# Performance work log

Measured on AMD Instinct MI355X. Metric: run time of the kernel, lower is better.

## Reference

```python
import jax, jax.numpy as jnp
import numpy as np

N = 100000   # nodes
E = 1600000  # edges
F = 128      # input/hidden dim
C = 3        # classes
G = 64       # graphs in batch


def setup_inputs() -> dict:
    key = jax.random.key(0)
    ks = jax.random.split(key, 12)
    s = 1.0 / np.sqrt(F)
    return {
        "x": jax.random.normal(ks[0], (N, F), dtype=jnp.float32),
        "edge_index": jax.random.randint(ks[1], (2, E), 0, N, dtype=jnp.int64),
        "batch": jnp.sort(jax.random.randint(ks[2], (N,), 0, G, dtype=jnp.int64)),
        "W1": jax.random.normal(ks[3], (F, F), dtype=jnp.float32) * s,
        "b1": jnp.zeros((F,), dtype=jnp.float32),
        "W2": jax.random.normal(ks[4], (F, F), dtype=jnp.float32) * s,
        "b2": jnp.zeros((F,), dtype=jnp.float32),
        "W3": jax.random.normal(ks[5], (F, F), dtype=jnp.float32) * s,
        "b3": jnp.zeros((F,), dtype=jnp.float32),
        "Wc": jax.random.normal(ks[6], (F, C), dtype=jnp.float32) * s,
        "bc": jnp.zeros((C,), dtype=jnp.float32),
    }


def reference(x, edge_index, batch, W1, b1, W2, b2, W3, b3, Wc, bc):
    n = x.shape[0]
    src, dst = edge_index[0], edge_index[1]
    # GCN adds self-loops: A_hat = A + I
    loops = jnp.arange(n, dtype=src.dtype)
    src_a = jnp.concatenate([src, loops])
    dst_a = jnp.concatenate([dst, loops])
    # symmetric normalization D^-1/2 (A+I) D^-1/2 (in-degree incl. self-loop)
    deg = jax.ops.segment_sum(jnp.ones_like(dst_a, dtype=x.dtype), dst_a, num_segments=n)
    dis = jnp.where(deg > 0, jax.lax.rsqrt(deg), 0.0)
    norm = dis[src_a] * dis[dst_a]  # [E+N]

    def gcn_conv(h, W, b):
        h = h @ W                                    # [N, F']
        msg = h[src_a] * norm[:, None]               # gather + scale
        agg = jax.ops.segment_sum(msg, dst_a, num_segments=n)  # scatter-add
        return agg + b

    h = jax.nn.relu(gcn_conv(x, W1, b1))   # dropout = identity in eval mode
    h = jax.nn.relu(gcn_conv(h, W2, b2))
    h = jax.nn.relu(gcn_conv(h, W3, b3))

    # global_mean_pool over graph ids
    sums = jax.ops.segment_sum(h, batch, num_segments=G)
    cnt = jax.ops.segment_sum(jnp.ones((n,), dtype=h.dtype), batch, num_segments=G)
    pooled = sums / jnp.maximum(cnt, 1.0)[:, None]
    return pooled @ Wc + bc
```

## Files before the change

### kernel.cpp

```cpp
#include <hip/hip_runtime.h>
#include <cstdint>
#include <cstddef>

#define FDIM 128
#define CHUNK 4096
#define BSHIFT 8
#define BMASK 255
#define MAXB 512

typedef unsigned short ushort_t;
typedef __attribute__((ext_vector_type(8))) short short8;
typedef __attribute__((ext_vector_type(4))) float floatx4;

__device__ inline ushort_t f2bf(float f) {
  unsigned u = __float_as_uint(f);
  u += 0x7fffu + ((u >> 16) & 1u);
  return (ushort_t)(u >> 16);
}
__device__ inline float bf2f(ushort_t h) {
  return __uint_as_float((unsigned)h << 16);
}

__global__ __launch_bounds__(256) void k_front(
    const float* __restrict__ x, const float* __restrict__ W1,
    const float* __restrict__ W2, const float* __restrict__ W3,
    ushort_t* __restrict__ h0, int n, int mmb,
    const int* __restrict__ dst, int e, int nb,
    int* __restrict__ chunkHist, int nch,
    ushort_t* __restrict__ wsw, int* __restrict__ counter,
    float* __restrict__ partials_g, int g_count) {
  __shared__ ushort_t Bs[16384];
  int tid = threadIdx.x;
  int bid = blockIdx.x;
  if (bid >= mmb) {
    int r = bid - mmb;
    if (r < nch) {
      int* h = (int*)Bs;
      int base = r * CHUNK;
      int end = min(base + CHUNK, e);
      for (int i = tid; i < nb; i += 256) h[i] = 0;
      __syncthreads();
      for (int i = base + tid; i < end; i += 256)
        atomicAdd(&h[dst[i] >> BSHIFT], 1);
      __syncthreads();
      for (int b = tid; b < nb; b += 256)
        chunkHist[(size_t)r * nb + b] = h[b];
      return;
    }
    int b = r - nch;
    if (b == 2) {
      for (int i = tid; i < g_count * FDIM; i += 256) partials_g[i] = 0.f;
      return;
    }
    if (b == 0 && tid == 0) *counter = 0;
    const float* W = (b == 0) ? W2 : W3;
    ushort_t* o = wsw + (size_t)b * 16384;
    for (int idx = tid; idx < 16384; idx += 256) {
      int j = idx & 7;
      int lane = (idx >> 3) & 63;
      int ct = (idx >> 9) & 7;
      int kc = idx >> 12;
      int k = kc * 32 + (lane >> 4) * 8 + j;
      int col = (lane & 15) * 8 + ct;
      o[idx] = f2bf(W[k * FDIM + col]);
    }
    return;
  }
  for (int q = tid; q < 2048; q += 256) {
    int lane = q & 63;
    int ct = (q >> 6) & 7;
    int kc = q >> 9;
    int col = (lane & 15) * 8 + ct;
    int kb = kc * 32 + (lane >> 4) * 8;
    unsigned t0 = f2bf(W1[(kb + 0) * FDIM + col]);
    unsigned t1 = f2bf(W1[(kb + 1) * FDIM + col]);
    unsigned t2 = f2bf(W1[(kb + 2) * FDIM + col]);
    unsigned t3 = f2bf(W1[(kb + 3) * FDIM + col]);
    unsigned t4 = f2bf(W1[(kb + 4) * FDIM + col]);
    unsigned t5 = f2bf(W1[(kb + 5) * FDIM + col]);
    unsigned t6 = f2bf(W1[(kb + 6) * FDIM + col]);
    unsigned t7 = f2bf(W1[(kb + 7) * FDIM + col]);
    uint4 pk;
    pk.x = t0 | (t1 << 16);
    pk.y = t2 | (t3 << 16);
    pk.z = t4 | (t5 << 16);
    pk.w = t6 | (t7 << 16);
    ((uint4*)Bs)[q] = pk;
  }
  __syncthreads();

  int w = tid >> 6;
  int lane = tid & 63;
  int quad = lane >> 4;
  int l15 = lane & 15;
  int rb = bid * 128 + w * 32;
  int row0 = rb + l15;
  int row1 = rb + 16 + l15;
  bool v0 = row0 < n, v1 = row1 < n;

  floatx4 acc[2][8];
#pragma unroll
  for (int rt = 0; rt < 2; ++rt)
#pragma unroll
    for (int ct = 0; ct < 8; ++ct) acc[rt][ct] = floatx4{0.f, 0.f, 0.f, 0.f};

#pragma unroll
  for (int kc = 0; kc < 4; ++kc) {
    int k0 = kc * 32 + quad * 8;
    short8 a0 = short8{0, 0, 0, 0, 0, 0, 0, 0};
    short8 a1 = short8{0, 0, 0, 0, 0, 0, 0, 0};
    if (v0) {
      float4 f0 = *(const float4*)&x[(size_t)row0 * FDIM + k0];
      float4 f1 = *(const float4*)&x[(size_t)row0 * FDIM + k0 + 4];
      a0 = short8{(short)f2bf(f0.x), (short)f2bf(f0.y), (short)f2bf(f0.z),
                  (short)f2bf(f0.w), (short)f2bf(f1.x), (short)f2bf(f1.y),
                  (short)f2bf(f1.z), (short)f2bf(f1.w)};
    }
    if (v1) {
      float4 f0 = *(const float4*)&x[(size_t)row1 * FDIM + k0];
      float4 f1 = *(const float4*)&x[(size_t)row1 * FDIM + k0 + 4];
      a1 = short8{(short)f2bf(f0.x), (short)f2bf(f0.y), (short)f2bf(f0.z),
                  (short)f2bf(f0.w), (short)f2bf(f1.x), (short)f2bf(f1.y),
                  (short)f2bf(f1.z), (short)f2bf(f1.w)};
    }
#pragma unroll
    for (int ct = 0; ct < 8; ++ct) {
      short8 bf = *(const short8*)&Bs[((kc * 8 + ct) * 64 + lane) * 8];
      acc[0][ct] = __builtin_amdgcn_mfma_f32_16x16x32_bf16(a0, bf, acc[0][ct], 0, 0, 0);
      acc[1][ct] = __builtin_amdgcn_mfma_f32_16x16x32_bf16(a1, bf, acc[1][ct], 0, 0, 0);
    }
  }
#pragma unroll
  for (int rt = 0; rt < 2; ++rt) {
#pragma unroll
    for (int i = 0; i < 4; ++i) {
      int row = rb + rt * 16 + quad * 4 + i;
      if (row < n) {
        uint4 pk;
        pk.x = (unsigned)f2bf(acc[rt][0][i]) | ((unsigned)f2bf(acc[rt][1][i]) << 16);
        pk.y = (unsigned)f2bf(acc[rt][2][i]) | ((unsigned)f2bf(acc[rt][3][i]) << 16);
        pk.z = (unsigned)f2bf(acc[rt][4][i]) | ((unsigned)f2bf(acc[rt][5][i]) << 16);
        pk.w = (unsigned)f2bf(acc[rt][6][i]) | ((unsigned)f2bf(acc[rt][7][i]) << 16);
        *(uint4*)&h0[(size_t)row * FDIM + l15 * 8] = pk;
      }
    }
  }
}

__global__ __launch_bounds__(512) void k_scan1(const int* __restrict__ chunkHist,
                                               int nchunks, int nb,
                                               int* __restrict__ chunkOff,
                                               int* __restrict__ bucketTotal,
                                               int* __restrict__ bucketBase,
                                               int* __restrict__ counter) {
  __shared__ int sb[512];
  int b = blockIdx.x;
  int t = threadIdx.x;
  int base = 0;
  for (int c0 = 0; c0 < nchunks; c0 += 512) {
    int c = c0 + t;
    int v = (c < nchunks) ? chunkHist[(size_t)c * nb + b] : 0;
    int x = v;
    sb[t] = x;
    __syncthreads();
    for (int off = 1; off < 512; off <<= 1) {
      int y = (t >= off) ? sb[t - off] : 0;
      __syncthreads();
      x += y;
      sb[t] = x;
      __syncthreads();
    }
    if (c < nchunks) chunkOff[(size_t)c * nb + b] = base + x - v;
    int tileTot = sb[511];
    __syncthreads();
    base += tileTot;
  }
  if (t == 0) {
    bucketTotal[b] = base;
    bucketBase[b] = atomicAdd(counter, base);
  }
}

__global__ __launch_bounds__(256) void k_bin(const int* __restrict__ src,
                                             const int* __restrict__ dst, int e, int nb,
                                             const int* __restrict__ chunkHist,
                                             const int* __restrict__ chunkOff,
                                             const int* __restrict__ bucketBase,
                                             unsigned* __restrict__ binned) {
  __shared__ unsigned sortedL[CHUNK];
  __shared__ int gtarget[CHUNK];
  __shared__ int lbase[MAXB], lcur[MAXB], gbase[MAXB];
  __shared__ int stmp[256];
  int c = blockIdx.x;
  int base = c * CHUNK;
  int end = min(base + CHUNK, e);
  for (int i = threadIdx.x; i < nb; i += 256) {
    lbase[i] = chunkHist[(size_t)c * nb + i];
    gbase[i] = bucketBase[i] + chunkOff[(size_t)c * nb + i];
  }
  __syncthreads();
  int carry = 0;
  for (int i0 = 0; i0 < nb; i0 += 256) {
    int i = i0 + threadIdx.x;
    int v = (i < nb) ? lbase[i] : 0;
    int x = v;
    stmp[threadIdx.x] = x;
    __syncthreads();
    for (int off = 1; off < 256; off <<= 1) {
      int y = (threadIdx.x >= off) ? stmp[threadIdx.x - off] : 0;
      __syncthreads();
      x += y;
      stmp[threadIdx.x] = x;
      __syncthreads();
    }
    if (i < nb) lbase[i] = carry + x - v;
    int tileTot = stmp[255];
    __syncthreads();
    carry += tileTot;
  }
  for (int i = threadIdx.x; i < nb; i += 256) lcur[i] = lbase[i];
  __syncthreads();
  for (int i = base + threadIdx.x; i < end; i += 256) {
    int d = dst[i];
    int sv = src[i];
    int b = d >> BSHIFT;
    int slot = atomicAdd(&lcur[b], 1);
    sortedL[slot] = ((unsigned)sv << BSHIFT) | (unsigned)(d & BMASK);
    gtarget[slot] = gbase[b] + (slot - lbase[b]);
  }
  __syncthreads();
  for (int i = threadIdx.x; i < end - base; i += 256)
    binned[gtarget[i]] = sortedL[i];
}

__global__ __launch_bounds__(256) void k_fill2(const unsigned* __restrict__ binned,
                                               const int* __restrict__ bucketBase,
                                               const int* __restrict__ bucketTotal,
                                               int n,
                                               int* __restrict__ rowStart,
                                               int* __restrict__ deg,
                                               float* __restrict__ dis,
                                               unsigned* __restrict__ colPacked) {
  __shared__ int h[256], sb[256], cur[256];
  int b = blockIdx.x;
  int s0 = bucketBase[b], s1 = s0 + bucketTotal[b];
  int nodeBase = b << BSHIFT;
  int t = threadIdx.x;
  h[t] = 0;
  __syncthreads();
  for (int i = s0 + t; i < s1; i += 256) atomicAdd(&h[binned[i] & BMASK], 1);
  __syncthreads();
  int v = h[t];
  int x = v;
  sb[t] = x;
  __syncthreads();
  for (int off = 1; off < 256; off <<= 1) {
    int y = (t >= off) ? sb[t - off] : 0;
    __syncthreads();
    x += y;
    sb[t] = x;
    __syncthreads();
  }
  int start = s0 + x - v;
  cur[t] = start;
  int node = nodeBase + t;
  if (node < n) {
    rowStart[node] = start;
    deg[node] = v;
    dis[node] = rsqrtf((float)(v + 1));
  }
  __syncthreads();
  for (int i = s0 + t; i < s1; i += 256) {
    unsigned en = binned[i];
    int slot = atomicAdd(&cur[en & BMASK], 1);
    colPacked[slot] = en >> BSHIFT;
  }
}

__global__ __launch_bounds__(256) void k_mm(const ushort_t* __restrict__ Ain,
                                            const ushort_t* __restrict__ Wsw,
                                            ushort_t* __restrict__ O, int n) {
  __shared__ ushort_t Bs[16384];
  int tid = threadIdx.x;
  for (int q = tid; q < 2048; q += 256)
    ((uint4*)Bs)[q] = ((const uint4*)Wsw)[q];
  __syncthreads();

  int w = tid >> 6;
  int lane = tid & 63;
  int quad = lane >> 4;
  int l15 = lane & 15;
  int rb = blockIdx.x * 128 + w * 32;

  int row0 = rb + l15;
  int row1 = rb + 16 + l15;
  bool v0 = row0 < n, v1 = row1 < n;

  floatx4 acc[2][8];
#pragma unroll
  for (int rt = 0; rt < 2; ++rt)
#pragma unroll
    for (int ct = 0; ct < 8; ++ct) acc[rt][ct] = floatx4{0.f, 0.f, 0.f, 0.f};

#pragma unroll
  for (int kc = 0; kc < 4; ++kc) {
    int k0 = kc * 32 + quad * 8;
    short8 a0 = short8{0, 0, 0, 0, 0, 0, 0, 0};
    short8 a1 = short8{0, 0, 0, 0, 0, 0, 0, 0};
    if (v0) a0 = *(const short8*)&Ain[(size_t)row0 * FDIM + k0];
    if (v1) a1 = *(const short8*)&Ain[(size_t)row1 * FDIM + k0];
#pragma unroll
    for (int ct = 0; ct < 8; ++ct) {
      short8 bf = *(const short8*)&Bs[((kc * 8 + ct) * 64 + lane) * 8];
      acc[0][ct] = __builtin_amdgcn_mfma_f32_16x16x32_bf16(a0, bf, acc[0][ct], 0, 0, 0);
      acc[1][ct] = __builtin_amdgcn_mfma_f32_16x16x32_bf16(a1, bf, acc[1][ct], 0, 0, 0);
    }
  }

#pragma unroll
  for (int rt = 0; rt < 2; ++rt) {
#pragma unroll
    for (int i = 0; i < 4; ++i) {
      int row = rb + rt * 16 + quad * 4 + i;
      if (row < n) {
        uint4 pk;
        pk.x = (unsigned)f2bf(acc[rt][0][i]) | ((unsigned)f2bf(acc[rt][1][i]) << 16);
        pk.y = (unsigned)f2bf(acc[rt][2][i]) | ((unsigned)f2bf(acc[rt][3][i]) << 16);
        pk.z = (unsigned)f2bf(acc[rt][4][i]) | ((unsigned)f2bf(acc[rt][5][i]) << 16);
        pk.w = (unsigned)f2bf(acc[rt][6][i]) | ((unsigned)f2bf(acc[rt][7][i]) << 16);
        *(uint4*)&O[(size_t)row * FDIM + l15 * 8] = pk;
      }
    }
  }
}

template <int POOL, int PACKED, int EDGW>
__global__ __launch_bounds__(256) void k_agg(const ushort_t* __restrict__ Hin,
                                             ushort_t* __restrict__ Hout,
                                             const int* __restrict__ rowStart,
                                             const int* __restrict__ degE,
                                             unsigned* __restrict__ colPacked,
                                             const float* __restrict__ dis,
                                             const float* __restrict__ bias, int n,
                                             int e,
                                             const int* __restrict__ batch,
                                             float* __restrict__ partials_blk,
                                             float* __restrict__ partials_g) {
  int tid = threadIdx.x;
  if (EDGW && blockIdx.x >= (unsigned)((n + 7) >> 3)) {
    int base = (blockIdx.x - ((n + 7) >> 3)) * 2048 + tid;
#pragma unroll
    for (int k = 0; k < 8; ++k) {
      int i = base + k * 256;
      if (i < e) {
        unsigned p = colPacked[i] & 0x1ffffu;
        colPacked[i] = p | ((unsigned)f2bf(dis[p]) << 17);
      }
    }
    return;
  }
  __shared__ float pool_s[POOL ? 4 * FDIM : 4];
  __shared__ int done;
  if (POOL) {
    if (tid == 0) done = 0;
    __syncthreads();
  }
  int node = blockIdx.x * 8 + (tid >> 5);
  int lane = tid & 31;
  bool act = node < n;
  if (!POOL && !act) return;
  float a0 = 0.f, a1 = 0.f, a2 = 0.f, a3 = 0.f;
  if (act) {
    const uint2* hin = (const uint2*)Hin;
    float di = dis[node];
    uint2 su = hin[(size_t)node * 32 + lane];
    float ws = di * di;
    a0 = ws * __uint_as_float(su.x << 16);
    a1 = ws * __uint_as_float(su.x & 0xffff0000u);
    a2 = ws * __uint_as_float(su.y << 16);
    a3 = ws * __uint_as_float(su.y & 0xffff0000u);
    int s0 = rowStart[node], cnt = degE[node];
    const unsigned* __restrict__ cp = colPacked + s0;

    int j = 0;
    int main8 = cnt & ~7;
    if (main8) {
      unsigned pv[8];
#pragma unroll
      for (int k = 0; k < 8; ++k) pv[k] = cp[k];
      for (;;) {
        float dv[8];
        uint2 u[8];
#pragma unroll
        for (int k = 0; k < 8; ++k) {
          unsigned sidx = pv[k] & 0x1ffffu;
          if (!PACKED) dv[k] = dis[(int)sidx];
          u[k] = hin[(size_t)sidx * 32 + lane];
        }
        int jn = j + 8;
        bool more = jn < main8;
        unsigned pn[8];
        if (more) {
#pragma unroll
          for (int k = 0; k < 8; ++k) pn[k] = cp[jn + k];
        }
#pragma unroll
        for (int k = 0; k < 8; ++k) {
          float w = PACKED ? di * __uint_as_float((pv[k] >> 17) << 16)
                           : di * dv[k];
          a0 += w * __uint_as_float(u[k].x << 16);
          a1 += w * __uint_as_float(u[k].x & 0xffff0000u);
          a2 += w * __uint_as_float(u[k].y << 16);
          a3 += w * __uint_as_float(u[k].y & 0xffff0000u);
        }
        j = jn;
        if (!more) break;
#pragma unroll
        for (int k = 0; k < 8; ++k) pv[k] = pn[k];
      }
    }
    if (j + 4 <= cnt) {
      unsigned pv[4];
#pragma unroll
      for (int k = 0; k < 4; ++k) pv[k] = cp[j + k];
      float dv[4];
      uint2 u[4];
#pragma unroll
      for (int k = 0; k < 4; ++k) {
        unsigned sidx = pv[k] & 0x1ffffu;
        if (!PACKED) dv[k] = dis[(int)sidx];
        u[k] = hin[(size_t)sidx * 32 + lane];
      }
#pragma unroll
      for (int k = 0; k < 4; ++k) {
        float w = PACKED ? di * __uint_as_float((pv[k] >> 17) << 16)
                         : di * dv[k];
        a0 += w * __uint_as_float(u[k].x << 16);
        a1 += w * __uint_as_float(u[k].x & 0xffff0000u);
        a2 += w * __uint_as_float(u[k].y << 16);
        a3 += w * __uint_as_float(u[k].y & 0xffff0000u);
      }
      j += 4;
    }
    for (; j < cnt; ++j) {
      unsigned pv = cp[j];
      unsigned sidx = pv & 0x1ffffu;
      float w = PACKED ? di * __uint_as_float((pv >> 17) << 16)
                       : di * dis[(int)sidx];
      uint2 u = hin[(size_t)sidx * 32 + lane];
      a0 += w * __uint_as_float(u.x << 16);
      a1 += w * __uint_as_float(u.x & 0xffff0000u);
      a2 += w * __uint_as_float(u.y << 16);
      a3 += w * __uint_as_float(u.y & 0xffff0000u);
    }
    float4 b = ((const float4*)bias)[lane];
    a0 = fmaxf(a0 + b.x, 0.f);
    a1 = fmaxf(a1 + b.y, 0.f);
    a2 = fmaxf(a2 + b.z, 0.f);
    a3 = fmaxf(a3 + b.w, 0.f);
    if (!POOL) {
      uint2 o;
      o.x = (unsigned)f2bf(a0) | ((unsigned)f2bf(a1) << 16);
      o.y = (unsigned)f2bf(a2) | ((unsigned)f2bf(a3) << 16);
      ((uint2*)Hout)[(size_t)node * 32 + lane] = o;
    }
  }
  if (POOL) {
    int base = blockIdx.x * 8;
    int lastn = min(base + 7, n - 1);
    int g0 = batch[base];
    int sg = (g0 == batch[lastn]) ? g0 : -1;
    int w = tid >> 6;
    int wl = tid & 63;
    int pl = wl ^ 32;
    float p0 = __shfl(a0, pl);
    float p1 = __shfl(a1, pl);
    float p2 = __shfl(a2, pl);
    float p3 = __shfl(a3, pl);
    if (sg >= 0) {
      if (wl < 32) {
        float4 v = {a0 + p0, a1 + p1, a2 + p2, a3 + p3};
        *(float4*)&pool_s[w * FDIM + wl * 4] = v;
      }
    } else {
      if (wl < 32) *(float4*)&pool_s[w * FDIM + wl * 4] = float4{0.f, 0.f, 0.f, 0.f};
      if (act) {
        int gn = batch[node];
        float* pg = &partials_g[(size_t)gn * FDIM + lane * 4];
        atomicAdd(pg + 0, a0);
        atomicAdd(pg + 1, a1);
        atomicAdd(pg + 2, a2);
        atomicAdd(pg + 3, a3);
      }
    }
    __threadfence_block();
    int old = 0;
    if (wl == 0) old = atomicAdd(&done, 1);
    old = __shfl(old, 0);
    if (old == 3) {
      int c = wl * 2;
      float s0 = 0.f, s1 = 0.f;
#pragma unroll
      for (int ww = 0; ww < 4; ++ww) {
        float2 v = *(float2*)&pool_s[ww * FDIM + c];
        s0 += v.x;
        s1 += v.y;
      }
      *(float2*)&partials_blk[(size_t)blockIdx.x * FDIM + c] = float2{s0, s1};
    }
  }
}


__device__ inline int lower_bound_batch(const int* __restrict__ batch, int n, int g) {
  int lo = 0, hi = n;
  while (lo < hi) {
    int mid = (lo + hi) >> 1;
    if (batch[mid] < g) lo = mid + 1;
    else hi = mid;
  }
  return lo;
}

__global__ __launch_bounds__(512) void k_final(const float* __restrict__ partials_blk,
                                               const float* __restrict__ partials_g,
                                               const int* __restrict__ batch, int n,
                                               const float* __restrict__ Wc,
                                               const float* __restrict__ bc,
                                               float* __restrict__ out, int g_count) {
  __shared__ float red2[4][FDIM];
  __shared__ int se[2];
  __shared__ float red[6];
  int t = threadIdx.x;
  int f = t & 127;
  int r = t >> 7;
  int g = blockIdx.x;
  if (t < 2) se[t] = lower_bound_batch(batch, n, g + t);
  __syncthreads();
  int s = se[0], e = se[1];
  float acc = (r == 0) ? partials_g[(size_t)g * FDIM + f] : 0.f;
  for (int b = ((s + 7) >> 3) + r; b * 8 < e; b += 4) {
    if (b * 8 + 8 <= e || e >= n)
      acc += partials_blk[(size_t)b * FDIM + f];
  }
  red2[r][f] = acc;
  __syncthreads();
  if (t < FDIM) {
    float sv = (red2[0][t] + red2[1][t] + red2[2][t] + red2[3][t]) /
               (float)max(e - s, 1);
#pragma unroll
    for (int c = 0; c < 3; ++c) {
      float v = sv * Wc[t * 3 + c];
#pragma unroll
      for (int off = 1; off < 64; off <<= 1) v += __shfl_xor(v, off);
      if ((t & 63) == 0) red[(t >> 6) * 3 + c] = v;
    }
  }
  __syncthreads();
  if (t < 3) out[g * 3 + t] = red[t] + red[3 + t] + bc[t];
}


extern "C" void kernel_launch(void* const* d_in, const int* in_sizes, int n_in,
                              void* d_out, int out_size, void* d_ws, size_t ws_size,
                              hipStream_t stream) {
  const float* x = (const float*)d_in[0];
  const int* edge = (const int*)d_in[1];
  const int* batch = (const int*)d_in[2];
  const float* W1 = (const float*)d_in[3];
  const float* b1 = (const float*)d_in[4];
  const float* W2 = (const float*)d_in[5];
  const float* b2 = (const float*)d_in[6];
  const float* W3 = (const float*)d_in[7];
  const float* b3 = (const float*)d_in[8];
  const float* Wc = (const float*)d_in[9];
  const float* bc = (const float*)d_in[10];
  float* out = (float*)d_out;

  const int N = in_sizes[0] / FDIM;
  const int E = in_sizes[1] / 2;
  const int G = out_size / 3;
  const int* src = edge;
  const int* dst = edge + E;

  const int NCH = (E + CHUNK - 1) / CHUNK;
  const int NB = (N + (1 << BSHIFT) - 1) >> BSHIFT;

  char* ws = (char*)d_ws;
  size_t off = 0;
  auto carve = [&](size_t bytes) -> void* {
    void* p = ws + off;
    off = (off + bytes + 255) & ~(size_t)255;
    return p;
  };
  int aggb = (N + 7) / 8;
  int ewb = (E + 2047) / 2048;
  ushort_t* h0 = (ushort_t*)carve((size_t)N * FDIM * 2);
  ushort_t* h1 = (ushort_t*)carve((size_t)N * FDIM * 2);
  unsigned* colPacked = (unsigned*)carve((size_t)E * 4);
  unsigned* binned = (unsigned*)carve((size_t)E * 4);
  int* chunkHist = (int*)carve((size_t)NCH * NB * 4);
  int* chunkOff = (int*)carve((size_t)NCH * NB * 4);
  int* bucketTotal = (int*)carve((size_t)NB * 4);
  int* bucketBase = (int*)carve((size_t)NB * 4);
  int* counter = (int*)carve(256);
  int* rowStart = (int*)carve((size_t)N * 4);
  int* deg = (int*)carve((size_t)N * 4);
  float* dis = (float*)carve((size_t)N * 4);
  float* partials_g = (float*)carve((size_t)G * FDIM * 4);
  float* partials_blk = (float*)carve((size_t)aggb * FDIM * 4);
  ushort_t* wsw = (ushort_t*)carve((size_t)2 * 16384 * 2);
  (void)n_in;
  (void)ws_size;

  int mmb = (N + 127) / 128;
  k_front<<<mmb + NCH + 3, 256, 0, stream>>>(x, W1, W2, W3, h0, N, mmb, dst, E, NB,
                                             chunkHist, NCH, wsw, counter,
                                             partials_g, G);
  k_scan1<<<NB, 512, 0, stream>>>(chunkHist, NCH, NB, chunkOff, bucketTotal,
                                  bucketBase, counter);
  k_bin<<<NCH, 256, 0, stream>>>(src, dst, E, NB, chunkHist, chunkOff, bucketBase,
                                 binned);
  k_fill2<<<NB, 256, 0, stream>>>(binned, bucketBase, bucketTotal, N, rowStart, deg,
                                  dis, colPacked);

  k_agg<0, 0, 1><<<aggb + ewb, 256, 0, stream>>>(h0, h1, rowStart, deg, colPacked,
                                                 dis, b1, N, E, nullptr, nullptr,
                                                 nullptr);
  k_mm<<<mmb, 256, 0, stream>>>(h1, wsw, h0, N);
  k_agg<0, 1, 0><<<aggb, 256, 0, stream>>>(h0, h1, rowStart, deg, colPacked, dis,
                                           b2, N, E, nullptr, nullptr, nullptr);
  k_mm<<<mmb, 256, 0, stream>>>(h1, wsw + 16384, h0, N);
  k_agg<1, 1, 0><<<aggb, 256, 0, stream>>>(h0, h1, rowStart, deg, colPacked, dis,
                                           b3, N, E, batch, partials_blk,
                                           partials_g);

  k_final<<<G, 512, 0, stream>>>(partials_blk, partials_g, batch, N, Wc, bc, out, G);
}
```

Measured before the change: 419.1 us.

## Fuse GCN layer kernels into a persistent megakernel with grid barriers

Replaces the separate aggregate, matmul, pooling and final kernels with one persistent kernel of 1024 blocks. Each block loops over virtual blocks, and the phases are separated by a two-level atomic grid barrier; k_front now also resets the barrier counters. The aim is to remove the launch and tail gaps between the six dependent kernels. In exchange, occupancy is capped at 4 blocks per CU for the memory-bound gather phases, and correctness relies on all 1024 blocks being co-resident, with only a timeout guard if they are not.

```diff
diff --git a/kernel.cpp b/kernel.cpp
--- a/kernel.cpp
+++ b/kernel.cpp
@@ -7,6 +7,7 @@
 #define BSHIFT 8
 #define BMASK 255
 #define MAXB 512
+#define GRIDB 1024
 
 typedef unsigned short ushort_t;
 typedef __attribute__((ext_vector_type(8))) short short8;
@@ -28,7 +29,7 @@
     const int* __restrict__ dst, int e, int nb,
     int* __restrict__ chunkHist, int nch,
     ushort_t* __restrict__ wsw, int* __restrict__ counter,
-    float* __restrict__ partials_g, int g_count) {
+    float* __restrict__ partials_g, int g_count, int* __restrict__ bar) {
   __shared__ ushort_t Bs[16384];
   int tid = threadIdx.x;
   int bid = blockIdx.x;
@@ -50,6 +51,7 @@
     int b = r - nch;
     if (b == 2) {
       for (int i = tid; i < g_count * FDIM; i += 256) partials_g[i] = 0.f;
+      if (tid < 64) bar[tid] = 0;
       return;
     }
     if (b == 0 && tid == 0) *counter = 0;
@@ -277,31 +279,71 @@
   }
 }
 
-__global__ __launch_bounds__(256) void k_mm(const ushort_t* __restrict__ Ain,
-                                            const ushort_t* __restrict__ Wsw,
-                                            ushort_t* __restrict__ O, int n) {
-  __shared__ ushort_t Bs[16384];
-  int tid = threadIdx.x;
+
+__device__ __forceinline__ void grid_sync(int* bar, int nblk, int expect, int bid) {
+  __syncthreads();
+  if (threadIdx.x == 0) {
+    __threadfence();
+    int leaf = bid & 31;
+    int lo = __hip_atomic_fetch_add(&bar[leaf], 1, __ATOMIC_RELAXED,
+                                    __HIP_MEMORY_SCOPE_AGENT);
+    if (lo == (nblk >> 5) - 1) {
+      __hip_atomic_store(&bar[leaf], 0, __ATOMIC_RELAXED, __HIP_MEMORY_SCOPE_AGENT);
+      int ro = __hip_atomic_fetch_add(&bar[32], 1, __ATOMIC_RELAXED,
+                                      __HIP_MEMORY_SCOPE_AGENT);
+      if (ro == 31) {
+        __hip_atomic_store(&bar[32], 0, __ATOMIC_RELAXED, __HIP_MEMORY_SCOPE_AGENT);
+        __hip_atomic_fetch_add(&bar[33], 1, __ATOMIC_RELEASE,
+                               __HIP_MEMORY_SCOPE_AGENT);
+      }
+    }
+    int guard = 0;
+    while (__hip_atomic_load(&bar[33], __ATOMIC_ACQUIRE,
+                             __HIP_MEMORY_SCOPE_AGENT) < expect &&
+           guard < (1 << 25)) {
+      __builtin_amdgcn_s_sleep(4);
+      ++guard;
+    }
+    __threadfence();
+  }
+  __syncthreads();
+}
+
+__device__ __forceinline__ void edgw_body(int rb, int tid,
+                                          unsigned* __restrict__ colPacked,
+                                          const float* __restrict__ dis, int e) {
+  int base = rb * 2048 + tid;
+#pragma unroll
+  for (int k = 0; k < 8; ++k) {
+    int i = base + k * 256;
+    if (i < e) {
+      unsigned p = colPacked[i] & 0x1ffffu;
+      colPacked[i] = p | ((unsigned)f2bf(dis[p]) << 17);
+    }
+  }
+}
+
+__device__ __forceinline__ void mm_body(int vb, int tid,
+                                        const ushort_t* __restrict__ Ain,
+                                        const ushort_t* __restrict__ Wsw,
+                                        ushort_t* __restrict__ O, int n,
+                                        ushort_t* Bs) {
   for (int q = tid; q < 2048; q += 256)
     ((uint4*)Bs)[q] = ((const uint4*)Wsw)[q];
   __syncthreads();
-
   int w = tid >> 6;
   int lane = tid & 63;
   int quad = lane >> 4;
   int l15 = lane & 15;
-  int rb = blockIdx.x * 128 + w * 32;
-
+  int rb = vb * 128 + w * 32;
   int row0 = rb + l15;
   int row1 = rb + 16 + l15;
   bool v0 = row0 < n, v1 = row1 < n;
-
   floatx4 acc[2][8];
 #pragma unroll
   for (int rt = 0; rt < 2; ++rt)
 #pragma unroll
     for (int ct = 0; ct < 8; ++ct) acc[rt][ct] = floatx4{0.f, 0.f, 0.f, 0.f};
-
 #pragma unroll
   for (int kc = 0; kc < 4; ++kc) {
     int k0 = kc * 32 + quad * 8;
@@ -316,7 +358,6 @@
       acc[1][ct] = __builtin_amdgcn_mfma_f32_16x16x32_bf16(a1, bf, acc[1][ct], 0, 0, 0);
     }
   }
-
 #pragma unroll
   for (int rt = 0; rt < 2; ++rt) {
 #pragma unroll
@@ -332,40 +373,18 @@
       }
     }
   }
-}
-
-template <int POOL, int PACKED, int EDGW>
-__global__ __launch_bounds__(256) void k_agg(const ushort_t* __restrict__ Hin,
-                                             ushort_t* __restrict__ Hout,
-                                             const int* __restrict__ rowStart,
-                                             const int* __restrict__ degE,
-                                             unsigned* __restrict__ colPacked,
-                                             const float* __restrict__ dis,
-                                             const float* __restrict__ bias, int n,
-                                             int e,
-                                             const int* __restrict__ batch,
-                                             float* __restrict__ partials_blk,
-                                             float* __restrict__ partials_g) {
-  int tid = threadIdx.x;
-  if (EDGW && blockIdx.x >= (unsigned)((n + 7) >> 3)) {
-    int base = (blockIdx.x - ((n + 7) >> 3)) * 2048 + tid;
-#pragma unroll
-    for (int k = 0; k < 8; ++k) {
-      int i = base + k * 256;
-      if (i < e) {
-        unsigned p = colPacked[i] & 0x1ffffu;
-        colPacked[i] = p | ((unsigned)f2bf(dis[p]) << 17);
-      }
-    }
-    return;
-  }
-  __shared__ float pool_s[POOL ? 4 * FDIM : 4];
-  __shared__ int done;
-  if (POOL) {
-    if (tid == 0) done = 0;
-    __syncthreads();
-  }
-  int node = blockIdx.x * 8 + (tid >> 5);
+  __syncthreads();
+}
+
+template <int POOL, int PACKED>
+__device__ __forceinline__ void agg_body(
+    int vb, int tid, const ushort_t* __restrict__ Hin,
+    ushort_t* __restrict__ Hout, const int* __restrict__ rowStart,
+    const int* __restrict__ degE, const unsigned* __restrict__ colPacked,
+    const float* __restrict__ dis, const float* __restrict__ bias, int n,
+    const int* __restrict__ batch, float* __restrict__ partials_blk,
+    float* __restrict__ partials_g, float* pool_sl, int* done_sl) {
+  int node = vb * 8 + (tid >> 5);
   int lane = tid & 31;
   bool act = node < n;
   if (!POOL && !act) return;
@@ -381,7 +400,6 @@
     a3 = ws * __uint_as_float(su.y & 0xffff0000u);
     int s0 = rowStart[node], cnt = degE[node];
     const unsigned* __restrict__ cp = colPacked + s0;
-
     int j = 0;
     int main8 = cnt & ~7;
     if (main8) {
@@ -406,8 +424,7 @@
         }
 #pragma unroll
         for (int k = 0; k < 8; ++k) {
-          float w = PACKED ? di * __uint_as_float((pv[k] >> 17) << 16)
-                           : di * dv[k];
+          float w = PACKED ? di * __uint_as_float((pv[k] >> 17) << 16) : di * dv[k];
           a0 += w * __uint_as_float(u[k].x << 16);
           a1 += w * __uint_as_float(u[k].x & 0xffff0000u);
           a2 += w * __uint_as_float(u[k].y << 16);
@@ -433,8 +450,7 @@
       }
 #pragma unroll
       for (int k = 0; k < 4; ++k) {
-        float w = PACKED ? di * __uint_as_float((pv[k] >> 17) << 16)
-                         : di * dv[k];
+        float w = PACKED ? di * __uint_as_float((pv[k] >> 17) << 16) : di * dv[k];
         a0 += w * __uint_as_float(u[k].x << 16);
         a1 += w * __uint_as_float(u[k].x & 0xffff0000u);
         a2 += w * __uint_as_float(u[k].y << 16);
@@ -466,7 +482,7 @@
     }
   }
   if (POOL) {
-    int base = blockIdx.x * 8;
+    int base = vb * 8;
     int lastn = min(base + 7, n - 1);
     int g0 = batch[base];
     int sg = (g0 == batch[lastn]) ? g0 : -1;
@@ -480,10 +496,10 @@
     if (sg >= 0) {
       if (wl < 32) {
         float4 v = {a0 + p0, a1 + p1, a2 + p2, a3 + p3};
-        *(float4*)&pool_s[w * FDIM + wl * 4] = v;
+        *(float4*)&pool_sl[w * FDIM + wl * 4] = v;
       }
     } else {
-      if (wl < 32) *(float4*)&pool_s[w * FDIM + wl * 4] = float4{0.f, 0.f, 0.f, 0.f};
+      if (wl < 32) *(float4*)&pool_sl[w * FDIM + wl * 4] = float4{0.f, 0.f, 0.f, 0.f};
       if (act) {
         int gn = batch[node];
         float* pg = &partials_g[(size_t)gn * FDIM + lane * 4];
@@ -495,22 +511,21 @@
     }
     __threadfence_block();
     int old = 0;
-    if (wl == 0) old = atomicAdd(&done, 1);
+    if (wl == 0) old = atomicAdd(done_sl, 1);
     old = __shfl(old, 0);
     if (old == 3) {
       int c = wl * 2;
-      float s0 = 0.f, s1 = 0.f;
+      float s0v = 0.f, s1v = 0.f;
 #pragma unroll
       for (int ww = 0; ww < 4; ++ww) {
-        float2 v = *(float2*)&pool_s[ww * FDIM + c];
-        s0 += v.x;
-        s1 += v.y;
-      }
-      *(float2*)&partials_blk[(size_t)blockIdx.x * FDIM + c] = float2{s0, s1};
-    }
-  }
-}
-
+        float2 v = *(float2*)&pool_sl[ww * FDIM + c];
+        s0v += v.x;
+        s1v += v.y;
+      }
+      *(float2*)&partials_blk[(size_t)vb * FDIM + c] = float2{s0v, s1v};
+    }
+  }
+}
 
 __device__ inline int lower_bound_batch(const int* __restrict__ batch, int n, int g) {
   int lo = 0, hi = n;
@@ -522,42 +537,97 @@
   return lo;
 }
 
-__global__ __launch_bounds__(512) void k_final(const float* __restrict__ partials_blk,
-                                               const float* __restrict__ partials_g,
-                                               const int* __restrict__ batch, int n,
-                                               const float* __restrict__ Wc,
-                                               const float* __restrict__ bc,
-                                               float* __restrict__ out, int g_count) {
-  __shared__ float red2[4][FDIM];
-  __shared__ int se[2];
-  __shared__ float red[6];
-  int t = threadIdx.x;
-  int f = t & 127;
-  int r = t >> 7;
-  int g = blockIdx.x;
-  if (t < 2) se[t] = lower_bound_batch(batch, n, g + t);
+__device__ __forceinline__ void final_body(int g, int tid,
+                                           const float* __restrict__ partials_blk,
+                                           const float* __restrict__ partials_g,
+                                           const int* __restrict__ batch, int n,
+                                           const float* __restrict__ Wc,
+                                           const float* __restrict__ bc,
+                                           float* __restrict__ out,
+                                           float (*red2)[FDIM], int* se,
+                                           float* red) {
+  if (tid < 2) se[tid] = lower_bound_batch(batch, n, g + tid);
   __syncthreads();
   int s = se[0], e = se[1];
+  int f = tid & 127;
+  int r = tid >> 7;
   float acc = (r == 0) ? partials_g[(size_t)g * FDIM + f] : 0.f;
-  for (int b = ((s + 7) >> 3) + r; b * 8 < e; b += 4) {
-    if (b * 8 + 8 <= e || e >= n)
-      acc += partials_blk[(size_t)b * FDIM + f];
+  for (int b = ((s + 7) >> 3) + r; b * 8 < e; b += 2) {
+    if (b * 8 + 8 <= e || e >= n) acc += partials_blk[(size_t)b * FDIM + f];
   }
   red2[r][f] = acc;
   __syncthreads();
-  if (t < FDIM) {
-    float sv = (red2[0][t] + red2[1][t] + red2[2][t] + red2[3][t]) /
-               (float)max(e - s, 1);
+  if (tid < FDIM) {
+    float sv = (red2[0][tid] + red2[1][tid]) / (float)max(e - s, 1);
 #pragma unroll
     for (int c = 0; c < 3; ++c) {
-      float v = sv * Wc[t * 3 + c];
+      float v = sv * Wc[tid * 3 + c];
 #pragma unroll
       for (int off = 1; off < 64; off <<= 1) v += __shfl_xor(v, off);
-      if ((t & 63) == 0) red[(t >> 6) * 3 + c] = v;
-    }
-  }
-  __syncthreads();
-  if (t < 3) out[g * 3 + t] = red[t] + red[3 + t] + bc[t];
+      if ((tid & 63) == 0) red[(tid >> 6) * 3 + c] = v;
+    }
+  }
+  __syncthreads();
+  if (tid < 3) out[g * 3 + tid] = red[tid] + red[3 + tid] + bc[tid];
+}
+
+__global__ __launch_bounds__(256, 4) void k_mega(
+    ushort_t* __restrict__ h0, ushort_t* __restrict__ h1,
+    const int* __restrict__ rowStart, const int* __restrict__ degE,
+    unsigned* __restrict__ colPacked, const float* __restrict__ dis,
+    const float* __restrict__ b1, const float* __restrict__ b2,
+    const float* __restrict__ b3, int n, int e, const int* __restrict__ batch,
+    float* __restrict__ partials_blk, float* __restrict__ partials_g,
+    const ushort_t* __restrict__ wsw, const float* __restrict__ Wc,
+    const float* __restrict__ bc, float* __restrict__ out, int g_count,
+    int* __restrict__ bar, int nblk) {
+  __shared__ union SMU {
+    ushort_t Bs[16384];
+    float pool[16][4][FDIM];
+    struct {
+      float red2[2][FDIM];
+      int se[2];
+      float red[6];
+    } fin;
+  } sm;
+  __shared__ int done[16];
+  int tid = threadIdx.x;
+  int bid = blockIdx.x;
+  int aggv = (n + 7) >> 3;
+  int mmv = (n + 127) >> 7;
+  int ewv = (e + 2047) >> 11;
+
+  for (int vb = bid; vb < aggv + ewv; vb += nblk) {
+    if (vb < aggv)
+      agg_body<0, 0>(vb, tid, h0, h1, rowStart, degE, colPacked, dis, b1, n,
+                     nullptr, nullptr, nullptr, nullptr, nullptr);
+    else
+      edgw_body(vb - aggv, tid, colPacked, dis, e);
+  }
+  grid_sync(bar, nblk, 1, bid);
+  for (int vb = bid; vb < mmv; vb += nblk)
+    mm_body(vb, tid, h1, wsw, h0, n, sm.Bs);
+  grid_sync(bar, nblk, 2, bid);
+  for (int vb = bid; vb < aggv; vb += nblk)
+    agg_body<0, 1>(vb, tid, h0, h1, rowStart, degE, colPacked, dis, b2, n,
+                   nullptr, nullptr, nullptr, nullptr, nullptr);
+  grid_sync(bar, nblk, 3, bid);
+  for (int vb = bid; vb < mmv; vb += nblk)
+    mm_body(vb, tid, h1, wsw + 16384, h0, n, sm.Bs);
+  grid_sync(bar, nblk, 4, bid);
+  if (tid < 16) done[tid] = 0;
+  __syncthreads();
+  {
+    int it = 0;
+    for (int vb = bid; vb < aggv; vb += nblk, ++it)
+      agg_body<1, 1>(vb, tid, h0, nullptr, rowStart, degE, colPacked, dis, b3,
+                     n, batch, partials_blk, partials_g, &sm.pool[it][0][0],
+                     &done[it]);
+  }
+  grid_sync(bar, nblk, 5, bid);
+  if (bid < g_count)
+    final_body(bid, tid, partials_blk, partials_g, batch, n, Wc, bc, out,
+               sm.fin.red2, sm.fin.se, sm.fin.red);
 }
 
 
@@ -594,7 +664,6 @@
     return p;
   };
   int aggb = (N + 7) / 8;
-  int ewb = (E + 2047) / 2048;
   ushort_t* h0 = (ushort_t*)carve((size_t)N * FDIM * 2);
   ushort_t* h1 = (ushort_t*)carve((size_t)N * FDIM * 2);
   unsigned* colPacked = (unsigned*)carve((size_t)E * 4);
@@ -604,6 +673,7 @@
   int* bucketTotal = (int*)carve((size_t)NB * 4);
   int* bucketBase = (int*)carve((size_t)NB * 4);
   int* counter = (int*)carve(256);
+  int* bar = (int*)carve(256);
   int* rowStart = (int*)carve((size_t)N * 4);
   int* deg = (int*)carve((size_t)N * 4);
   float* dis = (float*)carve((size_t)N * 4);
@@ -616,24 +686,14 @@
   int mmb = (N + 127) / 128;
   k_front<<<mmb + NCH + 3, 256, 0, stream>>>(x, W1, W2, W3, h0, N, mmb, dst, E, NB,
                                              chunkHist, NCH, wsw, counter,
-                                             partials_g, G);
+                                             partials_g, G, bar);
   k_scan1<<<NB, 512, 0, stream>>>(chunkHist, NCH, NB, chunkOff, bucketTotal,
                                   bucketBase, counter);
   k_bin<<<NCH, 256, 0, stream>>>(src, dst, E, NB, chunkHist, chunkOff, bucketBase,
                                  binned);
   k_fill2<<<NB, 256, 0, stream>>>(binned, bucketBase, bucketTotal, N, rowStart, deg,
                                   dis, colPacked);
-
-  k_agg<0, 0, 1><<<aggb + ewb, 256, 0, stream>>>(h0, h1, rowStart, deg, colPacked,
-                                                 dis, b1, N, E, nullptr, nullptr,
-                                                 nullptr);
-  k_mm<<<mmb, 256, 0, stream>>>(h1, wsw, h0, N);
-  k_agg<0, 1, 0><<<aggb, 256, 0, stream>>>(h0, h1, rowStart, deg, colPacked, dis,
-                                           b2, N, E, nullptr, nullptr, nullptr);
-  k_mm<<<mmb, 256, 0, stream>>>(h1, wsw + 16384, h0, N);
-  k_agg<1, 1, 0><<<aggb, 256, 0, stream>>>(h0, h1, rowStart, deg, colPacked, dis,
-                                           b3, N, E, batch, partials_blk,
-                                           partials_g);
-
-  k_final<<<G, 512, 0, stream>>>(partials_blk, partials_g, batch, N, Wc, bc, out, G);
-}
+  k_mega<<<GRIDB, 256, 0, stream>>>(h0, h1, rowStart, deg, colPacked, dis, b1, b2,
+                                    b3, N, E, batch, partials_blk, partials_g, wsw,
+                                    Wc, bc, out, G, bar, GRIDB);
+}
```

Result: slower. 1.225 ms (+192.2%).
